# Kernel optimization log

Measured on AMD Instinct MI355X. Metric: run time of the kernel, lower is better.

Reference implementation:

```python
import jax, jax.numpy as jnp
import numpy as np

B = 2048          # batch size
L = 8192          # number of fine-grained labels
G = 256           # meta_label_size (number of label groups)
BETA = 0.01       # config.beta


def setup_inputs() -> dict:
    key = jax.random.key(0)
    k1, k2, k3 = jax.random.split(key, 3)
    logits = jax.random.normal(k1, (B, L), dtype=jnp.float32)
    true_y = jax.random.randint(k2, (B, L), 0, 2, dtype=jnp.int32)
    group_ids = jax.random.randint(k3, (L,), 0, G, dtype=jnp.int32)
    return {"logits": logits, "true_y": true_y, "group_ids": group_ids}


def reference(logits, true_y, group_ids):
    # y_hat = sigmoid(logits); meta_prob[b, g] = prod_{l in group g} (1 - y_hat[b, l])
    # Using 1 - sigmoid(x) = sigmoid(-x):
    #   log meta_prob = segment_sum(log_sigmoid(-logits)) over labels per group.
    log_not = jax.nn.log_sigmoid(-logits)                                    # [B, L]
    grp_log = jax.ops.segment_sum(log_not.T, group_ids, num_segments=G).T    # [B, G]
    meta_probs = jnp.exp(grp_log)                                            # [B, G]

    # meta_y[b, g] = 1 if any true label of group g is set in row b (generate_meta_y)
    any_true = jax.ops.segment_sum(true_y.T.astype(jnp.float32), group_ids,
                                   num_segments=G).T                         # [B, G]
    meta_y = (any_true > 0).astype(logits.dtype)

    # BCELoss (mean reduction, torch clamps log terms at -100)
    log_p = jnp.maximum(grp_log, -100.0)
    log_1mp = jnp.maximum(jnp.log1p(-meta_probs), -100.0)
    bce = -jnp.mean(meta_y * log_p + (1.0 - meta_y) * log_1mp)
    return bce * BETA
```

## Files before the change

kernel.cpp:

```cpp
#include <hip/hip_runtime.h>
#include <math.h>

constexpr int   B_    = 2048;
constexpr int   L_    = 8192;
constexpr int   G_    = 256;
constexpr float BETA_ = 0.01f;
constexpr float BIG_  = 1024.0f;
constexpr int   PMAX  = L_ + G_ * 3;

__device__ __forceinline__ float log_sigmoid_neg(float x) {
    return -(fmaxf(x, 0.0f) + __logf(1.0f + __expf(-fabsf(x))));
}

extern "C" __global__ __launch_bounds__(1024)
void build_rank_kernel(const int* __restrict__ group_ids,
                       int* __restrict__ g_offs,
                       unsigned short* __restrict__ g_rank)
{
    __shared__ int s_hist[G_];
    __shared__ int s_scan[G_];
    __shared__ int s_cur[G_];

    const int t = threadIdx.x;

    if (t < G_) s_hist[t] = 0;

    int ids[8];
    #pragma unroll
    for (int i = 0; i < 8; ++i) ids[i] = group_ids[i * 1024 + t];

    __syncthreads();

    #pragma unroll
    for (int i = 0; i < 8; ++i) atomicAdd(&s_hist[ids[i]], 1);
    __syncthreads();

    if (t < G_) s_scan[t] = (s_hist[t] + 3) & ~3;
    __syncthreads();
    for (int off = 1; off < G_; off <<= 1) {
        int v = 0;
        if (t < G_ && t >= off) v = s_scan[t - off];
        __syncthreads();
        if (t < G_) s_scan[t] += v;
        __syncthreads();
    }

    if (t < G_) {
        const int excl = s_scan[t] - ((s_hist[t] + 3) & ~3);
        s_cur[t]  = excl;
        g_offs[t] = excl;
    }
    if (t == 0) g_offs[G_] = s_scan[G_ - 1];
    __syncthreads();

    #pragma unroll
    for (int i = 0; i < 8; ++i) {
        const int l = i * 1024 + t;
        g_rank[l] = (unsigned short)atomicAdd(&s_cur[ids[i]], 1);
    }
}

extern "C" __global__ __launch_bounds__(512, 8)
void meta_loss_kernel(const float* __restrict__ logits,
                      const int*   __restrict__ true_y,
                      const int*   __restrict__ g_offs,
                      const unsigned short* __restrict__ g_rank,
                      float*       __restrict__ out)
{
    __shared__ float s_row[PMAX];
    __shared__ float s_part[8];

    const int t = threadIdx.x;
    const int b = blockIdx.x;

    const float4*  lg = (const float4*)(logits + (size_t)b * L_);
    const int4*    ty = (const int4*)(true_y + (size_t)b * L_);
    const ushort4* rk = (const ushort4*)g_rank;
    float4* s_row4 = (float4*)s_row;

    int o0 = 0, o1 = 0;
    if (t < G_) { o0 = g_offs[t]; o1 = g_offs[t + 1]; }

    #pragma unroll
    for (int i = 0; i < 5; ++i) {
        const int j = i * 512 + t;
        if (j < PMAX / 4) s_row4[j] = make_float4(0.f, 0.f, 0.f, 0.f);
    }
    __syncthreads();

    #pragma unroll
    for (int i = 0; i < L_ / (4 * 512); ++i) {
        const int idx = i * 512 + t;
        const float4  x = lg[idx];
        const int4    y = ty[idx];
        const ushort4 r = rk[idx];
        s_row[r.x] = log_sigmoid_neg(x.x) + (y.x ? BIG_ : 0.0f);
        s_row[r.y] = log_sigmoid_neg(x.y) + (y.y ? BIG_ : 0.0f);
        s_row[r.z] = log_sigmoid_neg(x.z) + (y.z ? BIG_ : 0.0f);
        s_row[r.w] = log_sigmoid_neg(x.w) + (y.w ? BIG_ : 0.0f);
    }
    __syncthreads();

    float term = 0.0f;
    if (t < G_) {
        float4 a4 = make_float4(0.f, 0.f, 0.f, 0.f);
        for (int j = o0; j < o1; j += 4) {
            const float4 v = *(const float4*)&s_row[j];
            a4.x += v.x; a4.y += v.y; a4.z += v.z; a4.w += v.w;
        }
        const float enc = (a4.x + a4.y) + (a4.z + a4.w);

        const int   k  = __float2int_rn(enc * (1.0f / BIG_));
        const float gl = enc - BIG_ * (float)k;

        if (k != 0) {
            term = fmaxf(gl, -100.0f);
        } else {
            term = fmaxf(log1pf(-__expf(gl)), -100.0f);
        }
    }

    #pragma unroll
    for (int off = 32; off > 0; off >>= 1)
        term += __shfl_down(term, off, 64);
    if ((t & 63) == 0) s_part[t >> 6] = term;
    __syncthreads();

    if (t == 0) {
        float s = 0.0f;
        #pragma unroll
        for (int w = 0; w < 8; ++w) s += s_part[w];
        atomicAdd(out, s * (-BETA_ / ((float)B_ * (float)G_)));
    }
}

extern "C" void kernel_launch(void* const* d_in, const int* in_sizes, int n_in,
                              void* d_out, int out_size, void* d_ws, size_t ws_size,
                              hipStream_t stream) {
    const float* logits    = (const float*)d_in[0];
    const int*   true_y    = (const int*)d_in[1];
    const int*   group_ids = (const int*)d_in[2];
    float*       out       = (float*)d_out;

    int*            g_offs = (int*)d_ws;
    unsigned short* g_rank = (unsigned short*)((char*)d_ws + 2048);

    hipMemsetAsync(out, 0, sizeof(float), stream);

    build_rank_kernel<<<1, 1024, 0, stream>>>(group_ids, g_offs, g_rank);
    meta_loss_kernel<<<B_, 512, 0, stream>>>(logits, true_y, g_offs, g_rank, out);
}
```

Before: 50.70 us.

## Replace sorted-scatter segment sum with per-wave shared atomics and packed group ids

Drops the single-block counting-sort kernel that built group offsets and per-label ranks. Each row is now reduced with LDS float atomicAdd into four per-wavefront group accumulators, using group ids packed four per 32-bit word. The block shrinks to 256 threads, and the shared-memory footprint falls from about 36 KB to 4 KB. This removes the serial 1-block rank kernel and the padded scatter buffer, at the cost of LDS atomic contention and a summation order that is no longer deterministic.

```diff
diff --git a/kernel.cpp b/kernel.cpp
--- a/kernel.cpp
+++ b/kernel.cpp
@@ -6,130 +6,77 @@
 constexpr int   G_    = 256;
 constexpr float BETA_ = 0.01f;
 constexpr float BIG_  = 1024.0f;
-constexpr int   PMAX  = L_ + G_ * 3;
 
 __device__ __forceinline__ float log_sigmoid_neg(float x) {
     return -(fmaxf(x, 0.0f) + __logf(1.0f + __expf(-fabsf(x))));
 }
 
 extern "C" __global__ __launch_bounds__(1024)
-void build_rank_kernel(const int* __restrict__ group_ids,
-                       int* __restrict__ g_offs,
-                       unsigned short* __restrict__ g_rank)
+void pack_gid_kernel(const int* __restrict__ group_ids,
+                     unsigned int* __restrict__ gid8)
 {
-    __shared__ int s_hist[G_];
-    __shared__ int s_scan[G_];
-    __shared__ int s_cur[G_];
+    const int j = blockIdx.x * 1024 + threadIdx.x;
+    const int4 g = ((const int4*)group_ids)[j];
+    gid8[j] = (unsigned)(g.x & 255) | ((unsigned)(g.y & 255) << 8) |
+              ((unsigned)(g.z & 255) << 16) | ((unsigned)(g.w & 255) << 24);
+}
 
-    const int t = threadIdx.x;
+extern "C" __global__ __launch_bounds__(256, 8)
+void meta_loss_kernel(const float* __restrict__ logits,
+                      const int*   __restrict__ true_y,
+                      const unsigned int* __restrict__ gid8,
+                      float*       __restrict__ out)
+{
+    __shared__ float s_acc[4][G_];
+    __shared__ float s_part[4];
 
-    if (t < G_) s_hist[t] = 0;
+    const int t  = threadIdx.x;
+    const int b  = blockIdx.x;
+    const int wv = t >> 6;
 
-    int ids[8];
+    unsigned gbuf[8];
     #pragma unroll
-    for (int i = 0; i < 8; ++i) ids[i] = group_ids[i * 1024 + t];
+    for (int i = 0; i < 8; ++i) gbuf[i] = gid8[i * 256 + t];
 
+    ((float4*)s_acc)[t] = make_float4(0.f, 0.f, 0.f, 0.f);
     __syncthreads();
 
-    #pragma unroll
-    for (int i = 0; i < 8; ++i) atomicAdd(&s_hist[ids[i]], 1);
-    __syncthreads();
-
-    if (t < G_) s_scan[t] = (s_hist[t] + 3) & ~3;
-    __syncthreads();
-    for (int off = 1; off < G_; off <<= 1) {
-        int v = 0;
-        if (t < G_ && t >= off) v = s_scan[t - off];
-        __syncthreads();
-        if (t < G_) s_scan[t] += v;
-        __syncthreads();
-    }
-
-    if (t < G_) {
-        const int excl = s_scan[t] - ((s_hist[t] + 3) & ~3);
-        s_cur[t]  = excl;
-        g_offs[t] = excl;
-    }
-    if (t == 0) g_offs[G_] = s_scan[G_ - 1];
-    __syncthreads();
+    const float4* lg  = (const float4*)(logits + (size_t)b * L_);
+    const int4*   ty  = (const int4*)(true_y + (size_t)b * L_);
+    float*        acc = s_acc[wv];
 
     #pragma unroll
     for (int i = 0; i < 8; ++i) {
-        const int l = i * 1024 + t;
-        g_rank[l] = (unsigned short)atomicAdd(&s_cur[ids[i]], 1);
-    }
-}
-
-extern "C" __global__ __launch_bounds__(512, 8)
-void meta_loss_kernel(const float* __restrict__ logits,
-                      const int*   __restrict__ true_y,
-                      const int*   __restrict__ g_offs,
-                      const unsigned short* __restrict__ g_rank,
-                      float*       __restrict__ out)
-{
-    __shared__ float s_row[PMAX];
-    __shared__ float s_part[8];
-
-    const int t = threadIdx.x;
-    const int b = blockIdx.x;
-
-    const float4*  lg = (const float4*)(logits + (size_t)b * L_);
-    const int4*    ty = (const int4*)(true_y + (size_t)b * L_);
-    const ushort4* rk = (const ushort4*)g_rank;
-    float4* s_row4 = (float4*)s_row;
-
-    int o0 = 0, o1 = 0;
-    if (t < G_) { o0 = g_offs[t]; o1 = g_offs[t + 1]; }
-
-    #pragma unroll
-    for (int i = 0; i < 5; ++i) {
-        const int j = i * 512 + t;
-        if (j < PMAX / 4) s_row4[j] = make_float4(0.f, 0.f, 0.f, 0.f);
+        const int idx = i * 256 + t;
+        const float4   x  = lg[idx];
+        const int4     y  = ty[idx];
+        const unsigned g4 = gbuf[i];
+        atomicAdd(&acc[ g4        & 255u], log_sigmoid_neg(x.x) + (y.x ? BIG_ : 0.0f));
+        atomicAdd(&acc[(g4 >>  8) & 255u], log_sigmoid_neg(x.y) + (y.y ? BIG_ : 0.0f));
+        atomicAdd(&acc[(g4 >> 16) & 255u], log_sigmoid_neg(x.z) + (y.z ? BIG_ : 0.0f));
+        atomicAdd(&acc[ g4 >> 24        ], log_sigmoid_neg(x.w) + (y.w ? BIG_ : 0.0f));
     }
     __syncthreads();
 
-    #pragma unroll
-    for (int i = 0; i < L_ / (4 * 512); ++i) {
-        const int idx = i * 512 + t;
-        const float4  x = lg[idx];
-        const int4    y = ty[idx];
-        const ushort4 r = rk[idx];
-        s_row[r.x] = log_sigmoid_neg(x.x) + (y.x ? BIG_ : 0.0f);
-        s_row[r.y] = log_sigmoid_neg(x.y) + (y.y ? BIG_ : 0.0f);
-        s_row[r.z] = log_sigmoid_neg(x.z) + (y.z ? BIG_ : 0.0f);
-        s_row[r.w] = log_sigmoid_neg(x.w) + (y.w ? BIG_ : 0.0f);
-    }
-    __syncthreads();
+    const float enc = (s_acc[0][t] + s_acc[1][t]) + (s_acc[2][t] + s_acc[3][t]);
+    const int   k   = __float2int_rn(enc * (1.0f / BIG_));
+    const float gl  = enc - BIG_ * (float)k;
 
-    float term = 0.0f;
-    if (t < G_) {
-        float4 a4 = make_float4(0.f, 0.f, 0.f, 0.f);
-        for (int j = o0; j < o1; j += 4) {
-            const float4 v = *(const float4*)&s_row[j];
-            a4.x += v.x; a4.y += v.y; a4.z += v.z; a4.w += v.w;
-        }
-        const float enc = (a4.x + a4.y) + (a4.z + a4.w);
-
-        const int   k  = __float2int_rn(enc * (1.0f / BIG_));
-        const float gl = enc - BIG_ * (float)k;
-
-        if (k != 0) {
-            term = fmaxf(gl, -100.0f);
-        } else {
-            term = fmaxf(log1pf(-__expf(gl)), -100.0f);
-        }
+    float term;
+    if (k != 0) {
+        term = fmaxf(gl, -100.0f);
+    } else {
+        term = fmaxf(log1pf(-__expf(gl)), -100.0f);
     }
 
     #pragma unroll
     for (int off = 32; off > 0; off >>= 1)
         term += __shfl_down(term, off, 64);
-    if ((t & 63) == 0) s_part[t >> 6] = term;
+    if ((t & 63) == 0) s_part[wv] = term;
     __syncthreads();
 
     if (t == 0) {
-        float s = 0.0f;
-        #pragma unroll
-        for (int w = 0; w < 8; ++w) s += s_part[w];
+        const float s = (s_part[0] + s_part[1]) + (s_part[2] + s_part[3]);
         atomicAdd(out, s * (-BETA_ / ((float)B_ * (float)G_)));
     }
 }
@@ -142,11 +89,9 @@
     const int*   group_ids = (const int*)d_in[2];
     float*       out       = (float*)d_out;
 
-    int*            g_offs = (int*)d_ws;
-    unsigned short* g_rank = (unsigned short*)((char*)d_ws + 2048);
+    unsigned int* gid8 = (unsigned int*)d_ws;
 
     hipMemsetAsync(out, 0, sizeof(float), stream);
-
-    build_rank_kernel<<<1, 1024, 0, stream>>>(group_ids, g_offs, g_rank);
-    meta_loss_kernel<<<B_, 512, 0, stream>>>(logits, true_y, g_offs, g_rank, out);
+    pack_gid_kernel<<<2, 1024, 0, stream>>>(group_ids, gid8);
+    meta_loss_kernel<<<B_, 256, 0, stream>>>(logits, true_y, gid8, out);
 }
```

Result: slower. 103.2 us (+103.5%).

## Split each row across two blocks with per-half group ranks and finalize pass

Applied to the files above, without the earlier changes.

Each batch row is now processed by two 256-thread blocks, each covering half of the labels with its own group ranking and offsets. The per-group encoded sums are atomically accumulated into a B×G partial buffer, and a new finalize kernel decodes them and reduces to the loss. The goal is smaller shared memory per block for higher occupancy and better use of all 256 threads in the segment-reduce phase. In exchange it adds a 2 MB memset, global atomics, and an extra kernel launch.

```diff
diff --git a/kernel.cpp b/kernel.cpp
--- a/kernel.cpp
+++ b/kernel.cpp
@@ -6,7 +6,9 @@
 constexpr int   G_    = 256;
 constexpr float BETA_ = 0.01f;
 constexpr float BIG_  = 1024.0f;
-constexpr int   PMAX  = L_ + G_ * 3;
+
+constexpr int   HALF  = L_ / 2;
+constexpr int   PMAX  = HALF + G_ * 3;
 
 __device__ __forceinline__ float log_sigmoid_neg(float x) {
     return -(fmaxf(x, 0.0f) + __logf(1.0f + __expf(-fabsf(x))));
@@ -17,25 +19,25 @@
                        int* __restrict__ g_offs,
                        unsigned short* __restrict__ g_rank)
 {
-    __shared__ int s_hist[G_];
+    __shared__ int s_cnt[G_];
     __shared__ int s_scan[G_];
     __shared__ int s_cur[G_];
 
     const int t = threadIdx.x;
+    const int h = blockIdx.x;
 
-    if (t < G_) s_hist[t] = 0;
+    if (t < G_) s_cnt[t] = 0;
 
-    int ids[8];
-    #pragma unroll
-    for (int i = 0; i < 8; ++i) ids[i] = group_ids[i * 1024 + t];
-
+    const int4 ids = ((const int4*)group_ids)[h * 1024 + t];
     __syncthreads();
 
-    #pragma unroll
-    for (int i = 0; i < 8; ++i) atomicAdd(&s_hist[ids[i]], 1);
+    atomicAdd(&s_cnt[ids.x], 1);
+    atomicAdd(&s_cnt[ids.y], 1);
+    atomicAdd(&s_cnt[ids.z], 1);
+    atomicAdd(&s_cnt[ids.w], 1);
     __syncthreads();
 
-    if (t < G_) s_scan[t] = (s_hist[t] + 3) & ~3;
+    if (t < G_) s_scan[t] = (s_cnt[t] + 3) & ~3;
     __syncthreads();
     for (int off = 1; off < G_; off <<= 1) {
         int v = 0;
@@ -46,51 +48,52 @@
     }
 
     if (t < G_) {
-        const int excl = s_scan[t] - ((s_hist[t] + 3) & ~3);
-        s_cur[t]  = excl;
-        g_offs[t] = excl;
+        const int excl = s_scan[t] - ((s_cnt[t] + 3) & ~3);
+        s_cur[t] = excl;
+        g_offs[h * 257 + t] = excl;
     }
-    if (t == 0) g_offs[G_] = s_scan[G_ - 1];
+    if (t == 0) g_offs[h * 257 + G_] = s_scan[G_ - 1];
     __syncthreads();
 
-    #pragma unroll
-    for (int i = 0; i < 8; ++i) {
-        const int l = i * 1024 + t;
-        g_rank[l] = (unsigned short)atomicAdd(&s_cur[ids[i]], 1);
-    }
+    const int l = h * HALF + t * 4;
+    g_rank[l + 0] = (unsigned short)atomicAdd(&s_cur[ids.x], 1);
+    g_rank[l + 1] = (unsigned short)atomicAdd(&s_cur[ids.y], 1);
+    g_rank[l + 2] = (unsigned short)atomicAdd(&s_cur[ids.z], 1);
+    g_rank[l + 3] = (unsigned short)atomicAdd(&s_cur[ids.w], 1);
 }
 
-extern "C" __global__ __launch_bounds__(512, 8)
+
+extern "C" __global__ __launch_bounds__(256, 8)
 void meta_loss_kernel(const float* __restrict__ logits,
                       const int*   __restrict__ true_y,
                       const int*   __restrict__ g_offs,
                       const unsigned short* __restrict__ g_rank,
-                      float*       __restrict__ out)
+                      float*       __restrict__ partial)
 {
     __shared__ float s_row[PMAX];
-    __shared__ float s_part[8];
 
     const int t = threadIdx.x;
-    const int b = blockIdx.x;
+    const int b = blockIdx.x >> 1;
+    const int h = blockIdx.x & 1;
 
-    const float4*  lg = (const float4*)(logits + (size_t)b * L_);
-    const int4*    ty = (const int4*)(true_y + (size_t)b * L_);
-    const ushort4* rk = (const ushort4*)g_rank;
+    const float4*  lg = (const float4*)(logits + (size_t)b * L_ + h * HALF);
+    const int4*    ty = (const int4*)(true_y + (size_t)b * L_ + h * HALF);
+    const ushort4* rk = (const ushort4*)(g_rank + h * HALF);
     float4* s_row4 = (float4*)s_row;
 
-    int o0 = 0, o1 = 0;
-    if (t < G_) { o0 = g_offs[t]; o1 = g_offs[t + 1]; }
+    const int o0 = g_offs[h * 257 + t];
+    const int o1 = g_offs[h * 257 + t + 1];
 
     #pragma unroll
     for (int i = 0; i < 5; ++i) {
-        const int j = i * 512 + t;
+        const int j = i * 256 + t;
         if (j < PMAX / 4) s_row4[j] = make_float4(0.f, 0.f, 0.f, 0.f);
     }
     __syncthreads();
 
     #pragma unroll
-    for (int i = 0; i < L_ / (4 * 512); ++i) {
-        const int idx = i * 512 + t;
+    for (int i = 0; i < HALF / (4 * 256); ++i) {
+        const int idx = i * 256 + t;
         const float4  x = lg[idx];
         const int4    y = ty[idx];
         const ushort4 r = rk[idx];
@@ -101,23 +104,35 @@
     }
     __syncthreads();
 
-    float term = 0.0f;
-    if (t < G_) {
-        float4 a4 = make_float4(0.f, 0.f, 0.f, 0.f);
-        for (int j = o0; j < o1; j += 4) {
-            const float4 v = *(const float4*)&s_row[j];
-            a4.x += v.x; a4.y += v.y; a4.z += v.z; a4.w += v.w;
-        }
-        const float enc = (a4.x + a4.y) + (a4.z + a4.w);
+    float4 a4 = make_float4(0.f, 0.f, 0.f, 0.f);
+    for (int j = o0; j < o1; j += 4) {
+        const float4 v = *(const float4*)&s_row[j];
+        a4.x += v.x; a4.y += v.y; a4.z += v.z; a4.w += v.w;
+    }
+    const float enc = (a4.x + a4.y) + (a4.z + a4.w);
 
-        const int   k  = __float2int_rn(enc * (1.0f / BIG_));
-        const float gl = enc - BIG_ * (float)k;
+    if (o1 > o0)
+        atomicAdd(&partial[b * G_ + t], enc);
+}
 
-        if (k != 0) {
-            term = fmaxf(gl, -100.0f);
-        } else {
-            term = fmaxf(log1pf(-__expf(gl)), -100.0f);
-        }
+extern "C" __global__ __launch_bounds__(1024)
+void finalize_kernel(const float* __restrict__ partial,
+                     float* __restrict__ out)
+{
+    __shared__ float s_part[16];
+
+    const int t   = threadIdx.x;
+    const int idx = blockIdx.x * 1024 + t;
+
+    const float enc = partial[idx];
+    const int   k   = __float2int_rn(enc * (1.0f / BIG_));
+    const float gl  = enc - BIG_ * (float)k;
+
+    float term;
+    if (k != 0) {
+        term = fmaxf(gl, -100.0f);
+    } else {
+        term = fmaxf(log1pf(-__expf(gl)), -100.0f);
     }
 
     #pragma unroll
@@ -129,7 +144,7 @@
     if (t == 0) {
         float s = 0.0f;
         #pragma unroll
-        for (int w = 0; w < 8; ++w) s += s_part[w];
+        for (int w = 0; w < 16; ++w) s += s_part[w];
         atomicAdd(out, s * (-BETA_ / ((float)B_ * (float)G_)));
     }
 }
@@ -142,11 +157,14 @@
     const int*   group_ids = (const int*)d_in[2];
     float*       out       = (float*)d_out;
 
-    int*            g_offs = (int*)d_ws;
-    unsigned short* g_rank = (unsigned short*)((char*)d_ws + 2048);
+    float*          partial = (float*)d_ws;
+    unsigned short* g_rank  = (unsigned short*)((char*)d_ws + (size_t)B_ * G_ * 4);
+    int*            g_offs  = (int*)((char*)d_ws + (size_t)B_ * G_ * 4 + L_ * 2);
 
+    hipMemsetAsync(partial, 0, (size_t)B_ * G_ * 4, stream);
     hipMemsetAsync(out, 0, sizeof(float), stream);
 
-    build_rank_kernel<<<1, 1024, 0, stream>>>(group_ids, g_offs, g_rank);
-    meta_loss_kernel<<<B_, 512, 0, stream>>>(logits, true_y, g_offs, g_rank, out);
+    build_rank_kernel<<<2, 1024, 0, stream>>>(group_ids, g_offs, g_rank);
+    meta_loss_kernel<<<2 * B_, 256, 0, stream>>>(logits, true_y, g_offs, g_rank, partial);
+    finalize_kernel<<<(B_ * G_) / 1024, 1024, 0, stream>>>(partial, out);
 }
```

New measurement: 45.28 us. 1.12x faster.
